# Kernel optimization log

Hardware: AMD Instinct MI355X
Metric: run time of the kernel (lower is better)

## Reference

```python
import jax, jax.numpy as jnp
import numpy as np

B, N, T, D = 4, 128, 64, 768
L_ATTN, HEADS = 4, 8
M_SSM = 4
D_INNER, D_STATE, HEADDIM = 1536, 64, 64
NHEADS = D_INNER // HEADDIM  # 24
D_CONV = 4
CONV_DIM = D_INNER + 2 * D_STATE  # 1664
IN_PROJ = 2 * D_INNER + 2 * D_STATE + NHEADS  # 3224
FFN_MULT = 4


def rmsnorm(x, w, eps=1e-5):
    return x * jax.lax.rsqrt(jnp.mean(x * x, -1, keepdims=True) + eps) * w


def mha(q_in, kv_in, Wq, Wk, Wv, Wo):
    b, lq, d = q_in.shape
    lk = kv_in.shape[1]
    dh = d // HEADS
    scale = 1.0 / float(np.sqrt(dh))
    q = (q_in @ Wq).reshape(b, lq, HEADS, dh)
    k = (kv_in @ Wk).reshape(b, lk, HEADS, dh)
    v = (kv_in @ Wv).reshape(b, lk, HEADS, dh)
    scores = jnp.einsum('bqhd,bkhd->bhqk', q, k) * scale
    attn = jax.nn.softmax(scores, axis=-1)
    o = jnp.einsum('bhqk,bkhd->bqhd', attn, v).reshape(b, lq, d)
    return o @ Wo


def mamba_block(x, in_proj_w, conv_w, conv_b, dt_bias, A_log, D_skip, norm_w, out_proj_w):
    # x: (b, l, D); selective-scan (Mamba2) with scalar-per-head A, ngroups=1
    b, l, _ = x.shape
    zxbcdt = x @ in_proj_w                       # (b, l, IN_PROJ)
    z = zxbcdt[..., :D_INNER]
    xBC = zxbcdt[..., D_INNER:D_INNER + CONV_DIM]
    dt = zxbcdt[..., D_INNER + CONV_DIM:]        # (b, l, NHEADS)
    # causal depthwise conv1d, kernel D_CONV
    xp = jnp.pad(xBC, ((0, 0), (D_CONV - 1, 0), (0, 0)))
    xc = sum(conv_w[k] * xp[:, k:k + l] for k in range(D_CONV)) + conv_b
    xc = jax.nn.silu(xc)
    xs = xc[..., :D_INNER].reshape(b, l, NHEADS, HEADDIM)
    Bm = xc[..., D_INNER:D_INNER + D_STATE]      # (b, l, D_STATE)
    Cm = xc[..., D_INNER + D_STATE:]             # (b, l, D_STATE)
    dt = jax.nn.softplus(dt + dt_bias)           # (b, l, NHEADS)
    A = -jnp.exp(A_log)                          # (NHEADS,)
    h0 = jnp.zeros((b, NHEADS, HEADDIM, D_STATE), x.dtype)

    def step(h, inp):
        xt, Bt, Ct, dtt = inp                    # (b,nh,hd), (b,ds), (b,ds), (b,nh)
        dA = jnp.exp(dtt * A)                    # (b, nh)
        h = h * dA[:, :, None, None] + (dtt[:, :, None, None] * xt[..., None]) * Bt[:, None, None, :]
        y = jnp.einsum('bhps,bs->bhp', h, Ct)
        return h, y

    hT, ys = jax.lax.scan(step, h0, (xs.transpose(1, 0, 2, 3), Bm.transpose(1, 0, 2), Cm.transpose(1, 0, 2), dt.transpose(1, 0, 2)))
    y = ys.transpose(1, 0, 2, 3) + D_skip[:, None] * xs  # skip connection per head
    y = y.reshape(b, l, D_INNER)
    y = rmsnorm(y * jax.nn.silu(z), norm_w)      # gated RMSNorm
    return y @ out_proj_w, hT


def reference(precepts, actions, attn_norm1_w, Wq, Wk, Wv, Wo, attn_norm2_w, ffn_w1, ffn_b1, ffn_w2, ffn_b2, ssm_norm_w, in_proj_w, conv_w, conv_b, dt_bias, A_log, D_skip, mamba_norm_w, out_proj_w, proj_w, proj_b):
    p = precepts.reshape(B * N, T, D)
    a = actions.reshape(B * N, T, D)
    for i in range(L_ATTN):
        cross = (i + 1) % 2 == 0
        q = rmsnorm(p, attn_norm1_w[i])
        kv = a if cross else q
        p = p + mha(q, kv, Wq[i], Wk[i], Wv[i], Wo[i])
        h_ = rmsnorm(p, attn_norm2_w[i])
        p = p + (jax.nn.gelu(h_ @ ffn_w1[i] + ffn_b1[i]) @ ffn_w2[i] + ffn_b2[i])
    # (b n) t d -> (b t) n d : scan over the num_steps axis
    z = p.reshape(B, N, T, D).transpose(0, 2, 1, 3).reshape(B * T, N, D)
    h_last = None
    for m in range(M_SSM):
        out, h_last = mamba_block(rmsnorm(z, ssm_norm_w[m]), in_proj_w[m], conv_w[m], conv_b[m], dt_bias[m], A_log[m], D_skip[m], mamba_norm_w[m], out_proj_w[m])
        z = z + out
    y = z @ proj_w + proj_b
    y = y.reshape(B, T, N, D).transpose(0, 2, 1, 3)  # b n t d
    return y, h_last


def setup_inputs() -> dict:
    key = jax.random.key(0)
    ks = jax.random.split(key, 16)
    s = 0.02
    f32 = jnp.float32
    return {
        'precepts': jax.random.normal(ks[0], (B, N, T, D), f32),
        'actions': jax.random.normal(ks[1], (B, N, T, D), f32),
        'attn_norm1_w': jnp.ones((L_ATTN, D), f32),
        'Wq': s * jax.random.normal(ks[2], (L_ATTN, D, D), f32),
        'Wk': s * jax.random.normal(ks[3], (L_ATTN, D, D), f32),
        'Wv': s * jax.random.normal(ks[4], (L_ATTN, D, D), f32),
        'Wo': s * jax.random.normal(ks[5], (L_ATTN, D, D), f32),
        'attn_norm2_w': jnp.ones((L_ATTN, D), f32),
        'ffn_w1': s * jax.random.normal(ks[6], (L_ATTN, D, FFN_MULT * D), f32),
        'ffn_b1': jnp.zeros((L_ATTN, FFN_MULT * D), f32),
        'ffn_w2': s * jax.random.normal(ks[7], (L_ATTN, FFN_MULT * D, D), f32),
        'ffn_b2': jnp.zeros((L_ATTN, D), f32),
        'ssm_norm_w': jnp.ones((M_SSM, D), f32),
        'in_proj_w': s * jax.random.normal(ks[8], (M_SSM, D, IN_PROJ), f32),
        'conv_w': s * jax.random.normal(ks[9], (M_SSM, D_CONV, CONV_DIM), f32),
        'conv_b': jnp.zeros((M_SSM, CONV_DIM), f32),
        'dt_bias': jax.random.uniform(ks[10], (M_SSM, NHEADS), f32, -2.0, 0.0),
        'A_log': jnp.broadcast_to(jnp.log(jnp.arange(1, NHEADS + 1, dtype=f32)), (M_SSM, NHEADS)),
        'D_skip': jnp.ones((M_SSM, NHEADS), f32),
        'mamba_norm_w': jnp.ones((M_SSM, D_INNER), f32),
        'out_proj_w': s * jax.random.normal(ks[11], (M_SSM, D_INNER, D), f32),
        'proj_w': s * jax.random.normal(ks[12], (D, D), f32),
        'proj_b': jnp.zeros((D,), f32),
    }
```

## Files before the change

kernel.cpp:

```cpp
#include <hip/hip_runtime.h>
#include <hip/hip_bf16.h>
#include <math.h>

constexpr long TOK  = 32768;
constexpr long HALF = TOK * 768;
constexpr int FLAG_ACC = 1, FLAG_GELU = 2, FLAG_PERM = 4, FLAG_BF16 = 8;

typedef __bf16 bf16x8 __attribute__((ext_vector_type(8)));
typedef __bf16 bf16x4 __attribute__((ext_vector_type(4)));
typedef float  f32x4  __attribute__((ext_vector_type(4)));

__device__ __forceinline__ void gload_lds16(const void* g, void* l) {
    __builtin_amdgcn_global_load_lds(
        (const __attribute__((address_space(1))) void*)g,
        (__attribute__((address_space(3))) void*)l, 16, 0, 0);
}
__device__ __forceinline__ float bf2f(__hip_bfloat16 v) { return __bfloat162float(v); }

__global__ __launch_bounds__(512, 2) void gemm256(
    const __hip_bfloat16* __restrict__ A,
    const __hip_bfloat16* __restrict__ BT,
    const float* __restrict__ bias,
    void* __restrict__ Cv, int ldc,
    int M, int N, int K, int flags, int moff)
{
    __shared__ __hip_bfloat16 As[2][256 * 64];
    __shared__ __hip_bfloat16 Bs[2][256 * 64];
    const int tid = threadIdx.x;
    const int wid = tid >> 6, lane = tid & 63;
    const int wm = wid >> 2, wn = wid & 3;
    const int lrow = lane & 15, lk = lane >> 4;
    const int nwg = gridDim.x * gridDim.y;
    const int orig = blockIdx.y * gridDim.x + blockIdx.x;
    const int q8 = nwg >> 3, r8 = nwg & 7;
    const int xcd = orig & 7, off = orig >> 3;
    const int wgid = (xcd < r8 ? xcd * (q8 + 1) : r8 * (q8 + 1) + (xcd - r8) * q8) + off;
    const int bm = (wgid / gridDim.x) * 256, bn = (wgid % gridDim.x) * 256;
    const int nk = K >> 6;

    f32x4 acc[4][8];
#pragma unroll
    for (int nf = 0; nf < 4; nf++)
#pragma unroll
        for (int mf = 0; mf < 8; mf++) acc[nf][mf] = f32x4{0.f, 0.f, 0.f, 0.f};

    bf16x8 Af[4][2];
    bf16x8 B0[2][2];
    bf16x8 B1[2][2];

    auto stage = [&](int kt, int which) {
        if (kt >= nk) return;
        const int dbuf = kt & 1;
        __hip_bfloat16* lbase = (which >= 2 ? &Bs[dbuf][0] : &As[dbuf][0]) + (which & 1) * 8192;
        const __hip_bfloat16* g = (which >= 2 ? BT : A);
        const int trow = (which >= 2 ? bn : bm) + (which & 1) * 128;
#pragma unroll
        for (int i = 0; i < 2; i++) {
            const int slot = i * 512 + tid;
            const int rl = slot >> 3, ch = slot & 7;
            const int sc = (ch ^ (rl & 7)) * 8;
            const long src = (long)(trow + rl) * K + (long)kt * 64 + sc;
            char* l = (char*)lbase + (i * 512 + wid * 64) * 16;
            gload_lds16(g + src, l);
        }
    };
    auto readA = [&](int dbuf, int mh) {
#pragma unroll
        for (int mq = 0; mq < 4; mq++)
#pragma unroll
            for (int ks = 0; ks < 2; ks++) {
                const int r = wm * 128 + mh * 64 + mq * 16 + lrow;
                const int ch = ((ks * 4 + lk) ^ (r & 7)) * 8;
                Af[mq][ks] = *(const bf16x8*)(const void*)&As[dbuf][r * 64 + ch];
            }
    };
    auto readB0 = [&](int dbuf) {
#pragma unroll
        for (int nf = 0; nf < 2; nf++)
#pragma unroll
            for (int ks = 0; ks < 2; ks++) {
                const int r = wn * 64 + nf * 16 + lrow;
                const int ch = ((ks * 4 + lk) ^ (r & 7)) * 8;
                B0[nf][ks] = *(const bf16x8*)(const void*)&Bs[dbuf][r * 64 + ch];
            }
    };
    auto readB1 = [&](int dbuf) {
#pragma unroll
        for (int nf = 0; nf < 2; nf++)
#pragma unroll
            for (int ks = 0; ks < 2; ks++) {
                const int r = wn * 64 + (2 + nf) * 16 + lrow;
                const int ch = ((ks * 4 + lk) ^ (r & 7)) * 8;
                B1[nf][ks] = *(const bf16x8*)(const void*)&Bs[dbuf][r * 64 + ch];
            }
    };

    stage(0, 0); stage(0, 1); stage(0, 2); stage(0, 3);
    stage(1, 2); stage(1, 3);
    asm volatile("s_waitcnt vmcnt(4)" ::: "memory");
    __builtin_amdgcn_s_barrier();

    for (int kt = 0; kt < nk; kt++) {
        const int cur = kt & 1;
        readA(cur, 0); readB0(cur);
        stage(kt + 1, 0);
        __builtin_amdgcn_s_barrier();
        __builtin_amdgcn_s_setprio(1);
#pragma unroll
        for (int nf = 0; nf < 2; nf++)
#pragma unroll
            for (int mq = 0; mq < 4; mq++)
#pragma unroll
                for (int ks = 0; ks < 2; ks++)
                    acc[nf][mq] = __builtin_amdgcn_mfma_f32_16x16x32_bf16(B0[nf][ks], Af[mq][ks], acc[nf][mq], 0, 0, 0);
        __builtin_amdgcn_s_setprio(0);
        __builtin_amdgcn_s_barrier();
        readB1(cur);
        stage(kt + 1, 1);
        __builtin_amdgcn_s_barrier();
        __builtin_amdgcn_s_setprio(1);
#pragma unroll
        for (int nf = 0; nf < 2; nf++)
#pragma unroll
            for (int mq = 0; mq < 4; mq++)
#pragma unroll
                for (int ks = 0; ks < 2; ks++)
                    acc[2 + nf][mq] = __builtin_amdgcn_mfma_f32_16x16x32_bf16(B1[nf][ks], Af[mq][ks], acc[2 + nf][mq], 0, 0, 0);
        __builtin_amdgcn_s_setprio(0);
        __builtin_amdgcn_s_barrier();
        readA(cur, 1);
        stage(kt + 2, 2);
        __builtin_amdgcn_s_barrier();
        __builtin_amdgcn_s_setprio(1);
#pragma unroll
        for (int nf = 0; nf < 2; nf++)
#pragma unroll
            for (int mq = 0; mq < 4; mq++)
#pragma unroll
                for (int ks = 0; ks < 2; ks++)
                    acc[2 + nf][4 + mq] = __builtin_amdgcn_mfma_f32_16x16x32_bf16(B1[nf][ks], Af[mq][ks], acc[2 + nf][4 + mq], 0, 0, 0);
        __builtin_amdgcn_s_setprio(0);
        __builtin_amdgcn_s_barrier();
        stage(kt + 2, 3);
        if (kt + 2 < nk) asm volatile("s_waitcnt vmcnt(4)" ::: "memory");
        else             asm volatile("s_waitcnt vmcnt(0)" ::: "memory");
        __builtin_amdgcn_s_barrier();
        __builtin_amdgcn_s_setprio(1);
#pragma unroll
        for (int nf = 0; nf < 2; nf++)
#pragma unroll
            for (int mq = 0; mq < 4; mq++)
#pragma unroll
                for (int ks = 0; ks < 2; ks++)
                    acc[nf][4 + mq] = __builtin_amdgcn_mfma_f32_16x16x32_bf16(B0[nf][ks], Af[mq][ks], acc[nf][4 + mq], 0, 0, 0);
        __builtin_amdgcn_s_setprio(0);
        __builtin_amdgcn_s_barrier();
    }

    float* Cf = (float*)Cv;
    __hip_bfloat16* Cb = (__hip_bfloat16*)Cv;
#pragma unroll
    for (int nf = 0; nf < 4; nf++) {
        const int gcb = bn + wn * 64 + nf * 16 + lk * 4;
        if (gcb >= N) continue;
        f32x4 b4 = f32x4{0.f, 0.f, 0.f, 0.f};
        if (bias) b4 = *(const f32x4*)&bias[gcb];
#pragma unroll
        for (int mf = 0; mf < 8; mf++) {
            const int gr = bm + wm * 128 + mf * 16 + lrow;
            f32x4 v = acc[nf][mf] + b4;
            if (flags & FLAG_GELU) {
#pragma unroll
                for (int j = 0; j < 4; j++) {
                    const float x = v[j];
                    const float u = 1.5957691216057308f * (x + 0.044715f * x * x * x);
                    v[j] = x / (1.f + __expf(-u));
                }
            }
            if (flags & FLAG_PERM) {
                const int mg = moff + gr;
                const int b_ = mg >> 13, t_ = (mg >> 7) & 63, n_ = mg & 127;
                *(f32x4*)&Cf[(((long)(b_ * 128 + n_)) * 64 + t_) * ldc + gcb] = v;
            } else if (flags & FLAG_BF16) {
                __hip_bfloat16 o0 = __float2bfloat16(v[0]), o1 = __float2bfloat16(v[1]);
                __hip_bfloat16 o2 = __float2bfloat16(v[2]), o3 = __float2bfloat16(v[3]);
                ushort4 o = { *(ushort*)&o0, *(ushort*)&o1, *(ushort*)&o2, *(ushort*)&o3 };
                *(ushort4*)&Cb[(long)gr * ldc + gcb] = o;
            } else if (flags & FLAG_ACC) {
                float* dst = &Cf[(long)gr * ldc + gcb];
                f32x4 old = *(const f32x4*)dst;
                *(f32x4*)dst = old + v;
            } else {
                *(f32x4*)&Cf[(long)gr * ldc + gcb] = v;
            }
        }
    }
}

__global__ __launch_bounds__(256) void gemm_bf16(
    const __hip_bfloat16* __restrict__ A,
    const __hip_bfloat16* __restrict__ BT,
    const float* __restrict__ bias,
    void* __restrict__ Cv, int ldc,
    int M, int N, int K, int flags, int moff)
{
    __shared__ __hip_bfloat16 As[2][128 * 32];
    __shared__ __hip_bfloat16 Bs[2][128 * 32];
    const int tid = threadIdx.x;
    const int wv = tid >> 6, lane = tid & 63;
    const int nwg = gridDim.x * gridDim.y;
    const int orig = blockIdx.y * gridDim.x + blockIdx.x;
    const int q8 = nwg >> 3, r8 = nwg & 7;
    const int xcd = orig & 7, off = orig >> 3;
    const int wgid = (xcd < r8 ? xcd * (q8 + 1) : r8 * (q8 + 1) + (xcd - r8) * q8) + off;
    const int bm = (wgid / gridDim.x) * 128, bn = (wgid % gridDim.x) * 128;
    const int wr = (wv >> 1) * 64, wc = (wv & 1) * 64;
    const int lrow = lane & 15, lk = lane >> 4;
    const int ck = (lk ^ (lrow & 3) ^ ((lrow >> 2) & 3)) * 8;

    f32x4 acc[4][4];
#pragma unroll
    for (int n = 0; n < 4; n++)
#pragma unroll
        for (int m = 0; m < 4; m++) acc[n][m] = f32x4{0.f, 0.f, 0.f, 0.f};

    const int nk = K >> 5;
    auto stage = [&](int kt, int buf) {
#pragma unroll
        for (int i = 0; i < 2; i++) {
            const int lin = i * 256 + tid;
            const int row = lin >> 2;
            const int ks  = (((lin & 3) ^ (row & 3) ^ ((row >> 2) & 3)) * 8);
            const long asrc = (long)(bm + row) * K + kt * 32 + ks;
            const long bsrc = (long)(bn + row) * K + kt * 32 + ks;
            char* la = (char*)&As[buf][0] + (i * 256 + wv * 64) * 16;
            char* lb = (char*)&Bs[buf][0] + (i * 256 + wv * 64) * 16;
            gload_lds16(A + asrc, la);
            gload_lds16(BT + bsrc, lb);
        }
    };

    stage(0, 0);
    __syncthreads();
    for (int kt = 0; kt < nk; kt++) {
        const int cur = kt & 1;
        if (kt + 1 < nk) stage(kt + 1, cur ^ 1);
        bf16x8 af[4], bfr[4];
#pragma unroll
        for (int m = 0; m < 4; m++) {
            af[m]  = *(const bf16x8*)(const void*)&As[cur][(wr + m * 16 + lrow) * 32 + ck];
            bfr[m] = *(const bf16x8*)(const void*)&Bs[cur][(wc + m * 16 + lrow) * 32 + ck];
        }
#pragma unroll
        for (int n = 0; n < 4; n++)
#pragma unroll
            for (int m = 0; m < 4; m++)
                acc[n][m] = __builtin_amdgcn_mfma_f32_16x16x32_bf16(bfr[n], af[m], acc[n][m], 0, 0, 0);
        __syncthreads();
    }

    float* Cf = (float*)Cv;
    __hip_bfloat16* Cb = (__hip_bfloat16*)Cv;
#pragma unroll
    for (int n = 0; n < 4; n++) {
        const int gcb = bn + wc + n * 16 + lk * 4;
        if (gcb >= N) continue;
        f32x4 b4 = f32x4{0.f, 0.f, 0.f, 0.f};
        if (bias) b4 = *(const f32x4*)&bias[gcb];
#pragma unroll
        for (int m = 0; m < 4; m++) {
            const int gr = bm + wr + m * 16 + lrow;
            f32x4 v = acc[n][m] + b4;
            if (flags & FLAG_GELU) {
#pragma unroll
                for (int j = 0; j < 4; j++) {
                    const float x = v[j];
                    const float u = 1.5957691216057308f * (x + 0.044715f * x * x * x);
                    v[j] = x / (1.f + __expf(-u));
                }
            }
            if (flags & FLAG_PERM) {
                const int mg = moff + gr;
                const int b_ = mg >> 13, t_ = (mg >> 7) & 63, n_ = mg & 127;
                *(f32x4*)&Cf[(((long)(b_ * 128 + n_)) * 64 + t_) * ldc + gcb] = v;
            } else if (flags & FLAG_BF16) {
                __hip_bfloat16 o0 = __float2bfloat16(v[0]), o1 = __float2bfloat16(v[1]);
                __hip_bfloat16 o2 = __float2bfloat16(v[2]), o3 = __float2bfloat16(v[3]);
                ushort4 o = { *(ushort*)&o0, *(ushort*)&o1, *(ushort*)&o2, *(ushort*)&o3 };
                *(ushort4*)&Cb[(long)gr * ldc + gcb] = o;
            } else if (flags & FLAG_ACC) {
                float* dst = &Cf[(long)gr * ldc + gcb];
                f32x4 old = *(const f32x4*)dst;
                *(f32x4*)dst = old + v;
            } else {
                *(f32x4*)&Cf[(long)gr * ldc + gcb] = v;
            }
        }
    }
}

__global__ void convT_kernel(const float* __restrict__ W, __hip_bfloat16* __restrict__ WT,
                             int K, int N, int Npad)
{
    __shared__ float t[32][33];
    const int k0 = blockIdx.y * 32, n0 = blockIdx.x * 32;
    const int tx = threadIdx.x & 31, ty = threadIdx.x >> 5;
#pragma unroll
    for (int i = 0; i < 4; i++) {
        int k = k0 + ty + i * 8, n = n0 + tx;
        t[ty + i * 8][tx] = (k < K && n < N) ? W[(long)k * N + n] : 0.f;
    }
    __syncthreads();
#pragma unroll
    for (int i = 0; i < 4; i++) {
        int n = n0 + ty + i * 8, k = k0 + tx;
        if (n < Npad && k < K) WT[(long)n * K + k] = __float2bfloat16(t[tx][ty + i * 8]);
    }
}

__global__ void cvt_kernel(const float4* __restrict__ x, ushort4* __restrict__ y, long n4)
{
    long i = (long)blockIdx.x * 256 + threadIdx.x;
    if (i >= n4) return;
    float4 v = x[i];
    __hip_bfloat16 a = __float2bfloat16(v.x), b = __float2bfloat16(v.y);
    __hip_bfloat16 c = __float2bfloat16(v.z), d = __float2bfloat16(v.w);
    ushort4 o = { *(ushort*)&a, *(ushort*)&b, *(ushort*)&c, *(ushort*)&d };
    y[i] = o;
}

__global__ void rmsnorm_f32(const float* __restrict__ x, const float* __restrict__ w,
                            __hip_bfloat16* __restrict__ out, int D, int xs, int os, long nrows)
{
    const int wv = threadIdx.x >> 6, lane = threadIdx.x & 63;
    const long row = (long)blockIdx.x * 4 + wv;
    if (row >= nrows) return;
    const float* xr = x + row * xs;
    const int it = D >> 8;
    float ss = 0.f;
    for (int i = 0; i < it; i++) {
        const float4 v = *(const float4*)&xr[(i * 64 + lane) * 4];
        ss += v.x * v.x + v.y * v.y + v.z * v.z + v.w * v.w;
    }
    for (int o = 32; o; o >>= 1) ss += __shfl_xor(ss, o);
    const float sc = rsqrtf(ss / D + 1e-5f);
    __hip_bfloat16* orow = out + row * os;
    for (int i = 0; i < it; i++) {
        const int e = (i * 64 + lane) * 4;
        const float4 v = *(const float4*)&xr[e];
        const float4 g = *(const float4*)&w[e];
        bf16x4 o;
        o[0] = (__bf16)(v.x * sc * g.x); o[1] = (__bf16)(v.y * sc * g.y);
        o[2] = (__bf16)(v.z * sc * g.z); o[3] = (__bf16)(v.w * sc * g.w);
        *(bf16x4*)(void*)&orow[e] = o;
    }
}
__global__ void rmsnorm_b16(const __hip_bfloat16* __restrict__ x, const float* __restrict__ w,
                            __hip_bfloat16* __restrict__ out, int D, int xs, int os, long nrows)
{
    const int wv = threadIdx.x >> 6, lane = threadIdx.x & 63;
    const long row = (long)blockIdx.x * 4 + wv;
    if (row >= nrows) return;
    const __hip_bfloat16* xr = x + row * xs;
    const int it = D >> 8;
    float ss = 0.f;
    for (int i = 0; i < it; i++) {
        const bf16x4 v = *(const bf16x4*)(const void*)&xr[(i * 64 + lane) * 4];
#pragma unroll
        for (int e = 0; e < 4; e++) { const float f = (float)v[e]; ss += f * f; }
    }
    for (int o = 32; o; o >>= 1) ss += __shfl_xor(ss, o);
    const float sc = rsqrtf(ss / D + 1e-5f);
    __hip_bfloat16* orow = out + row * os;
    for (int i = 0; i < it; i++) {
        const int e = (i * 64 + lane) * 4;
        const bf16x4 v = *(const bf16x4*)(const void*)&xr[e];
        const float4 g = *(const float4*)&w[e];
        bf16x4 o;
        o[0] = (__bf16)((float)v[0] * sc * g.x); o[1] = (__bf16)((float)v[1] * sc * g.y);
        o[2] = (__bf16)((float)v[2] * sc * g.z); o[3] = (__bf16)((float)v[3] * sc * g.w);
        *(bf16x4*)(void*)&orow[e] = o;
    }
}

__global__ __launch_bounds__(256) void attn_kernel(
    const __hip_bfloat16* __restrict__ QKV, __hip_bfloat16* __restrict__ O)
{
    __shared__ __align__(16) __hip_bfloat16 Qs[3 * 64 * 32];
    __shared__ __align__(16) __hip_bfloat16 Ks[3 * 64 * 32];
    __shared__ __align__(16) __hip_bfloat16 VT[2 * 96 * 32];
    __shared__ __align__(16) __hip_bfloat16 Ps[2 * 64 * 32];
    const int tid = threadIdx.x;
    const int wid = tid >> 6, lane = tid & 63;
    const int lrow = lane & 15, lk = lane >> 4;
    const int b = blockIdx.x >> 3, h = blockIdx.x & 7;
    const long base = (long)b * 64 * 2304 + h * 96;

#pragma unroll
    for (int i = 0; i < 3; i++) {
        const int v = i * 256 + tid;
        const int r = v / 12, c8 = v - r * 12;
        const int kst = c8 >> 2, ch = c8 & 3, slot = ch ^ (r & 3);
        const bf16x8 q = *(const bf16x8*)(const void*)&QKV[base + (long)r * 2304 + c8 * 8];
        const bf16x8 k = *(const bf16x8*)(const void*)&QKV[base + (long)r * 2304 + 768 + c8 * 8];
        *(bf16x8*)(void*)&Qs[(kst * 64 + r) * 32 + slot * 8] = q;
        *(bf16x8*)(void*)&Ks[(kst * 64 + r) * 32 + slot * 8] = k;
    }
    for (int i = 0; i < 16; i++) {
        const int k = wid * 16 + i;
        const __hip_bfloat16* vrow = &QKV[base + (long)k * 2304 + 1536];
        const int sb = (k >> 3) & 3, khi = k >> 5, klo = k & 7;
        {
            const int d = lane;
            VT[(khi * 96 + d) * 32 + ((sb ^ (d & 3)) * 8) + klo] = vrow[d];
        }
        if (lane < 32) {
            const int d = 64 + lane;
            VT[(khi * 96 + d) * 32 + ((sb ^ (d & 3)) * 8) + klo] = vrow[d];
        }
    }
    __syncthreads();

    const int ck = (lk ^ (lrow & 3)) * 8;
    f32x4 s[4];
#pragma unroll
    for (int n = 0; n < 4; n++) s[n] = f32x4{0.f, 0.f, 0.f, 0.f};
#pragma unroll
    for (int kst = 0; kst < 3; kst++) {
        const bf16x8 qf = *(const bf16x8*)(const void*)&Qs[(kst * 64 + wid * 16 + lrow) * 32 + ck];
#pragma unroll
        for (int n = 0; n < 4; n++) {
            const bf16x8 kf = *(const bf16x8*)(const void*)&Ks[(kst * 64 + n * 16 + lrow) * 32 + ck];
            s[n] = __builtin_amdgcn_mfma_f32_16x16x32_bf16(qf, kf, s[n], 0, 0, 0);
        }
    }
    const float scale = 0.102062072615966f;
#pragma unroll
    for (int n = 0; n < 4; n++) s[n] *= scale;
    float inv[4];
#pragma unroll
    for (int j = 0; j < 4; j++) {
        float mx = fmaxf(fmaxf(s[0][j], s[1][j]), fmaxf(s[2][j], s[3][j]));
        mx = fmaxf(mx, __shfl_xor(mx, 1));
        mx = fmaxf(mx, __shfl_xor(mx, 2));
        mx = fmaxf(mx, __shfl_xor(mx, 4));
        mx = fmaxf(mx, __shfl_xor(mx, 8));
        float sum = 0.f;
#pragma unroll
        for (int n = 0; n < 4; n++) { s[n][j] = __expf(s[n][j] - mx); sum += s[n][j]; }
        sum += __shfl_xor(sum, 1);
        sum += __shfl_xor(sum, 2);
        sum += __shfl_xor(sum, 4);
        sum += __shfl_xor(sum, 8);
        inv[j] = 1.f / sum;
    }
#pragma unroll
    for (int n = 0; n < 4; n++) {
        const int k = n * 16 + lrow;
        const int kst = n >> 1, kc = ((n & 1) << 1) + (lrow >> 3), ke = lrow & 7;
#pragma unroll
        for (int j = 0; j < 4; j++) {
            const int q = wid * 16 + lk * 4 + j;
            Ps[(kst * 64 + q) * 32 + ((kc ^ (q & 3)) * 8) + ke] = __float2bfloat16(s[n][j] * inv[j]);
        }
    }
    __syncthreads();

    const int wq = wid >> 1, wd = wid & 1;
    f32x4 y[3][2];
#pragma unroll
    for (int mv = 0; mv < 3; mv++)
#pragma unroll
        for (int np = 0; np < 2; np++) y[mv][np] = f32x4{0.f, 0.f, 0.f, 0.f};
#pragma unroll
    for (int ks = 0; ks < 2; ks++) {
        bf16x8 vf[3], pf[2];
#pragma unroll
        for (int mv = 0; mv < 3; mv++)
            vf[mv] = *(const bf16x8*)(const void*)&VT[(ks * 96 + wd * 48 + mv * 16 + lrow) * 32 + ck];
#pragma unroll
        for (int np = 0; np < 2; np++)
            pf[np] = *(const bf16x8*)(const void*)&Ps[(ks * 64 + wq * 32 + np * 16 + lrow) * 32 + ck];
#pragma unroll
        for (int mv = 0; mv < 3; mv++)
#pragma unroll
            for (int np = 0; np < 2; np++)
                y[mv][np] = __builtin_amdgcn_mfma_f32_16x16x32_bf16(vf[mv], pf[np], y[mv][np], 0, 0, 0);
    }
#pragma unroll
    for (int mv = 0; mv < 3; mv++) {
        const int d0 = wd * 48 + mv * 16 + lk * 4;
#pragma unroll
        for (int np = 0; np < 2; np++) {
            const int q = wq * 32 + np * 16 + lrow;
            bf16x4 o;
#pragma unroll
            for (int j = 0; j < 4; j++) o[j] = (__bf16)y[mv][np][j];
            *(bf16x4*)(void*)&O[(long)(b * 64 + q) * 768 + h * 96 + d0] = o;
        }
    }
}

__global__ void transpose_kernel(const float* __restrict__ P, float* __restrict__ Z)
{
    long lin = (long)blockIdx.x * 256 + threadIdx.x;
    if (lin >= HALF) return;
    int d = (int)(lin % 768);
    long rowz = lin / 768;
    int n = rowz & 127, t = (int)((rowz >> 7) & 63), b = (int)(rowz >> 13);
    long rowp = ((long)(b * 128 + n)) * 64 + t;
    Z[lin] = P[rowp * 768 + d];
}

__global__ __launch_bounds__(256) void conv_kernel(
    const __hip_bfloat16* __restrict__ zx, const float* __restrict__ cw,
    const float* __restrict__ cb, __hip_bfloat16* __restrict__ xc,
    __hip_bfloat16* __restrict__ bcB, long rows)
{
    const long r = blockIdx.x;
    const int tid = threadIdx.x;
    if (tid >= 208) return;
    const int c0 = tid * 8;
    const int n = (int)(r & 127);
    float acc[8];
    {
        const float4 b0 = *(const float4*)&cb[c0];
        const float4 b1 = *(const float4*)&cb[c0 + 4];
        acc[0] = b0.x; acc[1] = b0.y; acc[2] = b0.z; acc[3] = b0.w;
        acc[4] = b1.x; acc[5] = b1.y; acc[6] = b1.z; acc[7] = b1.w;
    }
#pragma unroll
    for (int k = 0; k < 4; k++) {
        if (n - 3 + k < 0) continue;
        const bf16x8 xv = *(const bf16x8*)(const void*)&zx[(r - 3 + k) * 3328 + 1536 + c0];
        const float4 w0 = *(const float4*)&cw[k * 1664 + c0];
        const float4 w1 = *(const float4*)&cw[k * 1664 + c0 + 4];
        acc[0] += w0.x * (float)xv[0]; acc[1] += w0.y * (float)xv[1];
        acc[2] += w0.z * (float)xv[2]; acc[3] += w0.w * (float)xv[3];
        acc[4] += w1.x * (float)xv[4]; acc[5] += w1.y * (float)xv[5];
        acc[6] += w1.z * (float)xv[6]; acc[7] += w1.w * (float)xv[7];
    }
    bf16x8 o;
#pragma unroll
    for (int e = 0; e < 8; e++) {
        const float s = acc[e] / (1.f + __expf(-acc[e]));
        o[e] = (__bf16)s;
    }
    if (c0 < 1536) *(bf16x8*)(void*)&xc[r * 1664 + c0] = o;
    else           *(bf16x8*)(void*)&bcB[r * 128 + (c0 - 1536)] = o;
}

__global__ void dt_kernel(const __hip_bfloat16* __restrict__ zx, const float* __restrict__ bias,
                          float* __restrict__ dtf, long count)
{
    long lin = (long)blockIdx.x * 256 + threadIdx.x;
    if (lin >= count) return;
    int h = (int)(lin % 24);
    long r = lin / 24;
    float v = bf2f(zx[r * 3328 + 3200 + h]) + bias[h];
    dtf[lin] = (v > 0.f) ? v + log1pf(expf(-v)) : log1pf(expf(v));
}

__global__ __launch_bounds__(256) void ssd_kernel(
    const __hip_bfloat16* __restrict__ zx0, const float* __restrict__ dtf0,
    const __hip_bfloat16* __restrict__ bcB0, __hip_bfloat16* __restrict__ xc0,
    const float* __restrict__ Alog, const float* __restrict__ Dskip,
    float* __restrict__ hout, int bt0)
{
    __shared__ __align__(16) char SM[50688];
    __hip_bfloat16* Cl  = (__hip_bfloat16*)SM;
    __hip_bfloat16* Bl  = Cl + 8192;
    __hip_bfloat16* Ml  = (__hip_bfloat16*)SM;
    __hip_bfloat16* XTl = (__hip_bfloat16*)(SM + 32768);
    __hip_bfloat16* BTl = (__hip_bfloat16*)SM;
    float* cum = (float*)(SM + 49152);
    float* dtl = cum + 128;
    float* wl  = dtl + 128;

    const int tid = threadIdx.x;
    const int wid = tid >> 6, lane = tid & 63;
    const int lrow = lane & 15, lk = lane >> 4;
    const int btl = blockIdx.x / 24, h = blockIdx.x % 24;
    const long rowbase = (long)btl * 128;

    const __hip_bfloat16* zxp = zx0 + rowbase * 3328 + h * 64;
    const float* dtp = dtf0 + rowbase * 24;
    const __hip_bfloat16* bcp = bcB0 + rowbase * 128;
    __hip_bfloat16* xcp = xc0 + rowbase * 1664 + h * 64;

    const float A  = -expf(Alog[h]);
    const float Dh = Dskip[h];

#pragma unroll
    for (int i = 0; i < 4; i++) {
        const int v = tid + i * 256;
        const int row = v >> 3, c8 = v & 7;
        const int kst = c8 >> 2, ch = c8 & 3;
        const int slot = ch ^ (row & 3);
        bf16x8 vB = *(const bf16x8*)(const void*)&bcp[(long)row * 128 + c8 * 8];
        bf16x8 vC = *(const bf16x8*)(const void*)&bcp[(long)row * 128 + 64 + c8 * 8];
        *(bf16x8*)(void*)&Bl[(kst * 128 + row) * 32 + slot * 8] = vB;
        *(bf16x8*)(void*)&Cl[(kst * 128 + row) * 32 + slot * 8] = vC;
    }
    for (int i = 0; i < 32; i++) {
        const int t = wid * 32 + i;
        const int slot = (i >> 3) ^ (lane & 3);
        XTl[(wid * 64 + lane) * 32 + slot * 8 + (i & 7)] = xcp[(long)t * 1664 + lane];
    }
    if (tid < 128) dtl[tid] = dtp[(long)tid * 24 + h];
    __syncthreads();
    if (tid < 128) cum[tid] = dtl[tid] * A;
    __syncthreads();
    for (int off = 1; off < 128; off <<= 1) {
        float v = 0.f;
        if (tid < 128 && tid >= off) v = cum[tid - off];
        __syncthreads();
        if (tid < 128) cum[tid] += v;
        __syncthreads();
    }
    if (tid < 128) wl[tid] = expf(cum[127] - cum[tid]) * dtl[tid];
    __syncthreads();

    const int wr1 = (wid >> 1) * 64, wc1 = (wid & 1) * 64;
    const int ck = (lk ^ (lrow & 3)) * 8;
    f32x4 a1[4][4];
#pragma unroll
    for (int m = 0; m < 4; m++)
#pragma unroll
        for (int n = 0; n < 4; n++) a1[m][n] = f32x4{0.f, 0.f, 0.f, 0.f};
#pragma unroll
    for (int kst = 0; kst < 2; kst++) {
        bf16x8 ca[4], bb[4];
#pragma unroll
        for (int m = 0; m < 4; m++)
            ca[m] = *(const bf16x8*)(const void*)&Cl[(kst * 128 + wr1 + m * 16 + lrow) * 32 + ck];
#pragma unroll
        for (int n = 0; n < 4; n++)
            bb[n] = *(const bf16x8*)(const void*)&Bl[(kst * 128 + wc1 + n * 16 + lrow) * 32 + ck];
#pragma unroll
        for (int m = 0; m < 4; m++)
#pragma unroll
            for (int n = 0; n < 4; n++)
                a1[m][n] = __builtin_amdgcn_mfma_f32_16x16x32_bf16(ca[m], bb[n], a1[m][n], 0, 0, 0);
    }
    __syncthreads();

#pragma unroll
    for (int m = 0; m < 4; m++) {
        const int tb = wr1 + m * 16 + lk * 4;
        const f32x4 c4 = *(const f32x4*)&cum[tb];
#pragma unroll
        for (int n = 0; n < 4; n++) {
            const int j = wc1 + n * 16 + lrow;
            const float cj = cum[j], dj = dtl[j];
            const int jst = j >> 5, jc = (j >> 3) & 3, je = j & 7;
#pragma unroll
            for (int jj = 0; jj < 4; jj++) {
                const int t = tb + jj;
                float val = 0.f;
                if (j <= t) val = a1[m][n][jj] * expf(c4[jj] - cj) * dj;
                Ml[(jst * 128 + t) * 32 + ((jc ^ (t & 3)) * 8) + je] = __float2bfloat16(val);
            }
        }
    }
    __syncthreads();

    const int wr2 = (wid >> 1) * 64, wc2 = (wid & 1) * 32;
    f32x4 a2[4][2];
#pragma unroll
    for (int m = 0; m < 4; m++)
#pragma unroll
        for (int n = 0; n < 2; n++) a2[m][n] = f32x4{0.f, 0.f, 0.f, 0.f};
#pragma unroll
    for (int kst = 0; kst < 4; kst++) {
        bf16x8 am[4], bn[2];
#pragma unroll
        for (int m = 0; m < 4; m++)
            am[m] = *(const bf16x8*)(const void*)&Ml[(kst * 128 + wr2 + m * 16 + lrow) * 32 + ck];
#pragma unroll
        for (int n = 0; n < 2; n++)
            bn[n] = *(const bf16x8*)(const void*)&XTl[(kst * 64 + wc2 + n * 16 + lrow) * 32 + ck];
#pragma unroll
        for (int m = 0; m < 4; m++)
#pragma unroll
            for (int n = 0; n < 2; n++)
                a2[m][n] = __builtin_amdgcn_mfma_f32_16x16x32_bf16(am[m], bn[n], a2[m][n], 0, 0, 0);
    }

#pragma unroll
    for (int m = 0; m < 4; m++) {
        const int tb = wr2 + m * 16 + lk * 4;
#pragma unroll
        for (int n = 0; n < 2; n++) {
            const int p = wc2 + n * 16 + lrow;
#pragma unroll
            for (int jj = 0; jj < 4; jj++) {
                const int t = tb + jj;
                const float x = bf2f(XTl[((t >> 5) * 64 + p) * 32 + ((((t >> 3) & 3) ^ (p & 3)) * 8) + (t & 7)]);
                const float zg = bf2f(zxp[(long)t * 3328 + p]);
                const float y = (a2[m][n][jj] + Dh * x) * (zg / (1.f + expf(-zg)));
                xcp[(long)t * 1664 + p] = __float2bfloat16(y);
            }
        }
    }

    if (hout) {
        __syncthreads();
        for (int i = 0; i < 32; i++) {
            const int j = wid * 32 + i;
            const int slot = (i >> 3) ^ (lane & 3);
            BTl[(wid * 64 + lane) * 32 + slot * 8 + (j & 7)] = bcp[(long)j * 128 + lane];
        }
        __syncthreads();
        const int wrp = (wid >> 1) * 32, wcs = (wid & 1) * 32;
        f32x4 a3[2][2];
#pragma unroll
        for (int m = 0; m < 2; m++)
#pragma unroll
            for (int n = 0; n < 2; n++) a3[m][n] = f32x4{0.f, 0.f, 0.f, 0.f};
#pragma unroll
        for (int kst = 0; kst < 4; kst++) {
            const int jb = kst * 32 + lk * 8;
            const f32x4 wa = *(const f32x4*)&wl[jb];
            const f32x4 wb = *(const f32x4*)&wl[jb + 4];
            bf16x8 xw[2], bn[2];
#pragma unroll
            for (int m = 0; m < 2; m++) {
                bf16x8 xr = *(const bf16x8*)(const void*)&XTl[(kst * 64 + wrp + m * 16 + lrow) * 32 + ck];
                bf16x8 t;
#pragma unroll
                for (int e = 0; e < 4; e++) t[e] = (__bf16)((float)xr[e] * wa[e]);
#pragma unroll
                for (int e = 0; e < 4; e++) t[4 + e] = (__bf16)((float)xr[4 + e] * wb[e]);
                xw[m] = t;
            }
#pragma unroll
            for (int n = 0; n < 2; n++)
                bn[n] = *(const bf16x8*)(const void*)&BTl[(kst * 64 + wcs + n * 16 + lrow) * 32 + ck];
#pragma unroll
            for (int m = 0; m < 2; m++)
#pragma unroll
                for (int n = 0; n < 2; n++)
                    a3[m][n] = __builtin_amdgcn_mfma_f32_16x16x32_bf16(xw[m], bn[n], a3[m][n], 0, 0, 0);
        }
        float* hp = hout + ((long)(bt0 + btl) * 24 + h) * 4096;
#pragma unroll
        for (int m = 0; m < 2; m++) {
            const int pb = wrp + m * 16 + lk * 4;
#pragma unroll
            for (int n = 0; n < 2; n++) {
                const int s = wcs + n * 16 + lrow;
#pragma unroll
                for (int jj = 0; jj < 4; jj++)
                    hp[(long)(pb + jj) * 64 + s] = a3[m][n][jj];
            }
        }
    }
}

extern "C" void kernel_launch(void* const* d_in, const int* in_sizes, int n_in,
                              void* d_out, int out_size, void* d_ws, size_t ws_size,
                              hipStream_t stream)
{
    const float* precepts  = (const float*)d_in[0];
    const float* actions   = (const float*)d_in[1];
    const float* attn_n1   = (const float*)d_in[2];
    const float* Wq        = (const float*)d_in[3];
    const float* Wk        = (const float*)d_in[4];
    const float* Wv        = (const float*)d_in[5];
    const float* Wo        = (const float*)d_in[6];
    const float* attn_n2   = (const float*)d_in[7];
    const float* ffn_w1    = (const float*)d_in[8];
    const float* ffn_b1    = (const float*)d_in[9];
    const float* ffn_w2    = (const float*)d_in[10];
    const float* ffn_b2    = (const float*)d_in[11];
    const float* ssm_norm  = (const float*)d_in[12];
    const float* in_proj   = (const float*)d_in[13];
    const float* conv_w    = (const float*)d_in[14];
    const float* conv_b    = (const float*)d_in[15];
    const float* dt_bias   = (const float*)d_in[16];
    const float* A_log     = (const float*)d_in[17];
    const float* D_skip    = (const float*)d_in[18];
    const float* mamba_nw  = (const float*)d_in[19];
    const float* out_proj  = (const float*)d_in[20];
    const float* proj_w    = (const float*)d_in[21];
    const float* proj_b    = (const float*)d_in[22];

    float* out  = (float*)d_out;
    float* Z    = out;
    float* P    = out + HALF;
    float* hout = out + HALF;

    __hip_bfloat16* wb = (__hip_bfloat16*)d_ws;
    long wo = 0;
    auto walloc = [&](long els) { __hip_bfloat16* p = wb + wo; wo += els; return p; };
    __hip_bfloat16* WqkvT = walloc(4L * 2304 * 768);
    __hip_bfloat16* W1T   = walloc(4L * 3072 * 768);
    __hip_bfloat16* W2T   = walloc(4L * 768 * 3072);
    __hip_bfloat16* inT   = walloc(4L * 3328 * 768);
    __hip_bfloat16* outT  = walloc(4L * 768 * 1536);
    __hip_bfloat16* projT = walloc(768L * 768);
    __hip_bfloat16* WoT   = walloc(4L * 768 * 768);
    char* pbase = (char*)(wb + ((wo + 255) & ~255L));
    const size_t used_w = (size_t)(pbase - (char*)d_ws);
    const size_t avail = ws_size > used_w ? ws_size - used_w : 0;

    int CB = 512;
    while (CB > 8 && (unsigned long long)CB * 884736ull > avail) CB >>= 1;
    int CBT = 256;
    while (CBT > 2 && (unsigned long long)CBT * 1912832ull > avail) CBT >>= 1;

    auto gemm = [&](const __hip_bfloat16* A, const __hip_bfloat16* BT, const float* bias,
                    void* C, int ldc, int M, int N, int Npad, int K, int flags, int moff) {
        if ((M & 255) == 0 && (Npad & 255) == 0 && (K & 63) == 0) {
            dim3 g(Npad / 256, M / 256);
            hipLaunchKernelGGL(gemm256, g, dim3(512), 0, stream,
                               A, BT, bias, C, ldc, M, N, K, flags, moff);
        } else {
            dim3 g(Npad / 128, M / 128);
            hipLaunchKernelGGL(gemm_bf16, g, dim3(256), 0, stream,
                               A, BT, bias, C, ldc, M, N, K, flags, moff);
        }
    };
    auto cvtT = [&](const float* W, __hip_bfloat16* WT, int K, int N, int Npad) {
        dim3 g((Npad + 31) / 32, (K + 31) / 32);
        hipLaunchKernelGGL(convT_kernel, g, dim3(256), 0, stream, W, WT, K, N, Npad);
    };
    auto cvt = [&](const float* x, __hip_bfloat16* y, long n) {
        long n4 = n / 4;
        hipLaunchKernelGGL(cvt_kernel, dim3((n4 + 255) / 256), dim3(256), 0, stream,
                           (const float4*)x, (ushort4*)y, n4);
    };
    auto rmsF = [&](const float* x, const float* w, __hip_bfloat16* o, int D, int xs, int os, long rows) {
        hipLaunchKernelGGL(rmsnorm_f32, dim3((rows + 3) / 4), dim3(256), 0, stream,
                           x, w, o, D, xs, os, rows);
    };
    auto rmsB = [&](const __hip_bfloat16* x, const float* w, __hip_bfloat16* o, int D, int xs, int os, long rows) {
        hipLaunchKernelGGL(rmsnorm_b16, dim3((rows + 3) / 4), dim3(256), 0, stream,
                           x, w, o, D, xs, os, rows);
    };

    for (int l = 0; l < 4; l++) {
        cvtT(Wq + (long)l * 589824, WqkvT + (long)l * 2304 * 768,                768, 768, 768);
        cvtT(Wk + (long)l * 589824, WqkvT + (long)l * 2304 * 768 +  768L * 768,  768, 768, 768);
        cvtT(Wv + (long)l * 589824, WqkvT + (long)l * 2304 * 768 + 1536L * 768,  768, 768, 768);
        cvtT(Wo + (long)l * 589824, WoT + (long)l * 589824, 768, 768, 768);
        cvtT(ffn_w1 + (long)l * 2359296, W1T + (long)l * 2359296, 768, 3072, 3072);
        cvtT(ffn_w2 + (long)l * 2359296, W2T + (long)l * 2359296, 3072, 768, 768);
    }
    for (int m = 0; m < 4; m++) {
        cvtT(in_proj + (long)m * 768 * 3224, inT + (long)m * 3328 * 768, 768, 3224, 3328);
        cvtT(out_proj + (long)m * 1536 * 768, outT + (long)m * 768 * 1536, 1536, 768, 768);
    }
    cvtT(proj_w, projT, 768, 768, 768);

    hipMemcpyAsync(P, precepts, HALF * sizeof(float), hipMemcpyDeviceToDevice, stream);
    {
        const long rA = (long)CB * 64;
        __hip_bfloat16* bufA   = (__hip_bfloat16*)pbase;
        __hip_bfloat16* actB   = bufA + rA * 768;
        __hip_bfloat16* bufQKV = actB + rA * 768;
        __hip_bfloat16* bufH   = bufQKV + rA * 2304;
        const int nac = 512 / CB;
        const int Mr = (int)rA;
        if (nac == 1) cvt(actions, actB, rA * 768);
        for (int layer = 0; layer < 4; layer++) {
            const bool cross = ((layer + 1) % 2) == 0;
            for (int c = 0; c < nac; c++) {
                const long tok0 = (long)c * rA;
                float* Pc = P + tok0 * 768;
                rmsF(Pc, attn_n1 + layer * 768, bufA, 768, 768, 768, Mr);
                if (!cross) {
                    gemm(bufA, WqkvT + (long)layer * 2304 * 768, nullptr, bufQKV, 2304,
                         Mr, 2304, 2304, 768, FLAG_BF16, 0);
                } else {
                    if (nac != 1) cvt(actions + tok0 * 768, actB, rA * 768);
                    gemm(bufA, WqkvT + (long)layer * 2304 * 768, nullptr, bufQKV, 2304,
                         Mr, 768, 768, 768, FLAG_BF16, 0);
                    gemm(actB, WqkvT + (long)layer * 2304 * 768 + 768L * 768, nullptr,
                         bufQKV + 768, 2304, Mr, 1536, 1536, 768, FLAG_BF16, 0);
                }
                hipLaunchKernelGGL(attn_kernel, dim3(CB * 8), dim3(256), 0, stream,
                                   bufQKV, bufA);
                gemm(bufA, WoT + (long)layer * 589824, nullptr, Pc, 768,
                     Mr, 768, 768, 768, FLAG_ACC, 0);
                rmsF(Pc, attn_n2 + layer * 768, bufA, 768, 768, 768, Mr);
                gemm(bufA, W1T + (long)layer * 2359296, ffn_b1 + layer * 3072, bufH, 3072,
                     Mr, 3072, 3072, 768, FLAG_GELU | FLAG_BF16, 0);
                gemm(bufH, W2T + (long)layer * 2359296, ffn_b2 + layer * 768, Pc, 768,
                     Mr, 768, 768, 3072, FLAG_ACC, 0);
            }
        }
    }

    hipLaunchKernelGGL(transpose_kernel, dim3((int)((HALF + 255) / 256)), dim3(256), 0, stream, P, Z);

    {
        const long rM = (long)CBT * 128;
        __hip_bfloat16* xn  = (__hip_bfloat16*)pbase;
        __hip_bfloat16* zx  = xn + rM * 768;
        float*          dtf = (float*)(zx + rM * 3328);
        __hip_bfloat16* xc  = (__hip_bfloat16*)(dtf + rM * 24);
        __hip_bfloat16* yb  = xc + rM * 1664;
        __hip_bfloat16* bcB = yb + rM * 1536;
        const int nmc = 256 / CBT;
        const int Mr = (int)rM;
        for (int m = 0; m < 4; m++) {
            for (int c = 0; c < nmc; c++) {
                float* Zc = Z + (long)c * rM * 768;
                rmsF(Zc, ssm_norm + m * 768, xn, 768, 768, 768, Mr);
                gemm(xn, inT + (long)m * 3328 * 768, nullptr, zx, 3328,
                     Mr, 3224, 3328, 768, FLAG_BF16, 0);
                hipLaunchKernelGGL(conv_kernel, dim3((int)rM), dim3(256), 0, stream,
                                   zx, conv_w + m * 4 * 1664, conv_b + m * 1664, xc, bcB, rM);
                const long dtn = rM * 24;
                hipLaunchKernelGGL(dt_kernel, dim3((int)((dtn + 255) / 256)), dim3(256), 0, stream,
                                   zx, dt_bias + m * 24, dtf, dtn);
                hipLaunchKernelGGL(ssd_kernel, dim3(CBT * 24), dim3(256), 0, stream,
                                   zx, dtf, bcB, xc, A_log + m * 24, D_skip + m * 24,
                                   (m == 3) ? hout : nullptr, c * CBT);
                rmsB(xc, mamba_nw + m * 1536, yb, 1536, 1664, 1536, Mr);
                gemm(yb, outT + (long)m * 768 * 1536, nullptr, Zc, 768,
                     Mr, 768, 768, 1536, FLAG_ACC, 0);
            }
        }
    }

    {
        __hip_bfloat16* Zb = (__hip_bfloat16*)pbase;
        cvt(Z, Zb, HALF);
        gemm(Zb, projT, proj_b, out, 768, 32768, 768, 768, 768, FLAG_PERM, 0);
    }
}
```

Measured before the change: 7.152 ms.

## Stage bf16 GEMM epilogue through LDS for coalesced stores; regroup prefetch and MFMA order

For bf16 outputs the epilogue now writes each wave's converted tile into a padded region of shared memory and then reads it back as full 16-byte rows, so global stores are coalesced instead of scattered 8-byte writes. The main loop also issues two stage prefetches together in the first phase and reorders the MFMA loop nest to put the k-slice outermost. The epilogue reuses the A shared buffer, which assumes every wave has finished its last reads; there is no barrier before the writes, and the N bounds check is dropped on the bf16 path.

```diff
diff --git a/kernel.cpp b/kernel.cpp
--- a/kernel.cpp
+++ b/kernel.cpp
@@ -24,8 +24,8 @@
     void* __restrict__ Cv, int ldc,
     int M, int N, int K, int flags, int moff)
 {
-    __shared__ __hip_bfloat16 As[2][256 * 64];
-    __shared__ __hip_bfloat16 Bs[2][256 * 64];
+    __shared__ __align__(16) __hip_bfloat16 As[2][256 * 64];
+    __shared__ __align__(16) __hip_bfloat16 Bs[2][256 * 64];
     const int tid = threadIdx.x;
     const int wid = tid >> 6, lane = tid & 63;
     const int wm = wid >> 2, wn = wid & 3;
@@ -103,28 +103,27 @@
     for (int kt = 0; kt < nk; kt++) {
         const int cur = kt & 1;
         readA(cur, 0); readB0(cur);
-        stage(kt + 1, 0);
+        stage(kt + 1, 0); stage(kt + 1, 1);
         __builtin_amdgcn_s_barrier();
         __builtin_amdgcn_s_setprio(1);
 #pragma unroll
-        for (int nf = 0; nf < 2; nf++)
-#pragma unroll
-            for (int mq = 0; mq < 4; mq++)
-#pragma unroll
-                for (int ks = 0; ks < 2; ks++)
+        for (int ks = 0; ks < 2; ks++)
+#pragma unroll
+            for (int nf = 0; nf < 2; nf++)
+#pragma unroll
+                for (int mq = 0; mq < 4; mq++)
                     acc[nf][mq] = __builtin_amdgcn_mfma_f32_16x16x32_bf16(B0[nf][ks], Af[mq][ks], acc[nf][mq], 0, 0, 0);
         __builtin_amdgcn_s_setprio(0);
         __builtin_amdgcn_s_barrier();
         readB1(cur);
-        stage(kt + 1, 1);
         __builtin_amdgcn_s_barrier();
         __builtin_amdgcn_s_setprio(1);
 #pragma unroll
-        for (int nf = 0; nf < 2; nf++)
-#pragma unroll
-            for (int mq = 0; mq < 4; mq++)
-#pragma unroll
-                for (int ks = 0; ks < 2; ks++)
+        for (int ks = 0; ks < 2; ks++)
+#pragma unroll
+            for (int nf = 0; nf < 2; nf++)
+#pragma unroll
+                for (int mq = 0; mq < 4; mq++)
                     acc[2 + nf][mq] = __builtin_amdgcn_mfma_f32_16x16x32_bf16(B1[nf][ks], Af[mq][ks], acc[2 + nf][mq], 0, 0, 0);
         __builtin_amdgcn_s_setprio(0);
         __builtin_amdgcn_s_barrier();
@@ -133,11 +132,11 @@
         __builtin_amdgcn_s_barrier();
         __builtin_amdgcn_s_setprio(1);
 #pragma unroll
-        for (int nf = 0; nf < 2; nf++)
-#pragma unroll
-            for (int mq = 0; mq < 4; mq++)
-#pragma unroll
-                for (int ks = 0; ks < 2; ks++)
+        for (int ks = 0; ks < 2; ks++)
+#pragma unroll
+            for (int nf = 0; nf < 2; nf++)
+#pragma unroll
+                for (int mq = 0; mq < 4; mq++)
                     acc[2 + nf][4 + mq] = __builtin_amdgcn_mfma_f32_16x16x32_bf16(B1[nf][ks], Af[mq][ks], acc[2 + nf][4 + mq], 0, 0, 0);
         __builtin_amdgcn_s_setprio(0);
         __builtin_amdgcn_s_barrier();
@@ -147,11 +146,11 @@
         __builtin_amdgcn_s_barrier();
         __builtin_amdgcn_s_setprio(1);
 #pragma unroll
-        for (int nf = 0; nf < 2; nf++)
-#pragma unroll
-            for (int mq = 0; mq < 4; mq++)
-#pragma unroll
-                for (int ks = 0; ks < 2; ks++)
+        for (int ks = 0; ks < 2; ks++)
+#pragma unroll
+            for (int nf = 0; nf < 2; nf++)
+#pragma unroll
+                for (int mq = 0; mq < 4; mq++)
                     acc[nf][4 + mq] = __builtin_amdgcn_mfma_f32_16x16x32_bf16(B0[nf][ks], Af[mq][ks], acc[nf][4 + mq], 0, 0, 0);
         __builtin_amdgcn_s_setprio(0);
         __builtin_amdgcn_s_barrier();
@@ -159,39 +158,74 @@
 
     float* Cf = (float*)Cv;
     __hip_bfloat16* Cb = (__hip_bfloat16*)Cv;
-#pragma unroll
-    for (int nf = 0; nf < 4; nf++) {
-        const int gcb = bn + wn * 64 + nf * 16 + lk * 4;
-        if (gcb >= N) continue;
-        f32x4 b4 = f32x4{0.f, 0.f, 0.f, 0.f};
-        if (bias) b4 = *(const f32x4*)&bias[gcb];
-#pragma unroll
-        for (int mf = 0; mf < 8; mf++) {
-            const int gr = bm + wm * 128 + mf * 16 + lrow;
-            f32x4 v = acc[nf][mf] + b4;
-            if (flags & FLAG_GELU) {
-#pragma unroll
-                for (int j = 0; j < 4; j++) {
-                    const float x = v[j];
-                    const float u = 1.5957691216057308f * (x + 0.044715f * x * x * x);
-                    v[j] = x / (1.f + __expf(-u));
+    if (flags & FLAG_BF16) {
+        char* lw = (char*)&As[0][0] + (size_t)wid * (64 * 176);
+        const int colg = bn + wn * 64;
+#pragma unroll
+        for (int half = 0; half < 2; half++) {
+#pragma unroll
+            for (int nf = 0; nf < 4; nf++) {
+                const int col = nf * 16 + lk * 4;
+                f32x4 b4 = f32x4{0.f, 0.f, 0.f, 0.f};
+                if (bias) b4 = *(const f32x4*)&bias[colg + col];
+#pragma unroll
+                for (int m4 = 0; m4 < 4; m4++) {
+                    const int row = m4 * 16 + lrow;
+                    f32x4 v = acc[nf][half * 4 + m4] + b4;
+                    if (flags & FLAG_GELU) {
+#pragma unroll
+                        for (int j = 0; j < 4; j++) {
+                            const float x = v[j];
+                            const float u = 1.5957691216057308f * (x + 0.044715f * x * x * x);
+                            v[j] = x / (1.f + __expf(-u));
+                        }
+                    }
+                    bf16x4 o;
+                    o[0] = (__bf16)v[0]; o[1] = (__bf16)v[1];
+                    o[2] = (__bf16)v[2]; o[3] = (__bf16)v[3];
+                    *(bf16x4*)(void*)(lw + row * 176 + col * 2) = o;
                 }
             }
-            if (flags & FLAG_PERM) {
-                const int mg = moff + gr;
-                const int b_ = mg >> 13, t_ = (mg >> 7) & 63, n_ = mg & 127;
-                *(f32x4*)&Cf[(((long)(b_ * 128 + n_)) * 64 + t_) * ldc + gcb] = v;
-            } else if (flags & FLAG_BF16) {
-                __hip_bfloat16 o0 = __float2bfloat16(v[0]), o1 = __float2bfloat16(v[1]);
-                __hip_bfloat16 o2 = __float2bfloat16(v[2]), o3 = __float2bfloat16(v[3]);
-                ushort4 o = { *(ushort*)&o0, *(ushort*)&o1, *(ushort*)&o2, *(ushort*)&o3 };
-                *(ushort4*)&Cb[(long)gr * ldc + gcb] = o;
-            } else if (flags & FLAG_ACC) {
-                float* dst = &Cf[(long)gr * ldc + gcb];
-                f32x4 old = *(const f32x4*)dst;
-                *(f32x4*)dst = old + v;
-            } else {
-                *(f32x4*)&Cf[(long)gr * ldc + gcb] = v;
+            asm volatile("s_waitcnt lgkmcnt(0)" ::: "memory");
+#pragma unroll
+            for (int rr = 0; rr < 8; rr++) {
+                const int row = rr * 8 + (lane >> 3);
+                const long gr = (long)(bm + wm * 128 + half * 64 + row);
+                const bf16x8 d = *(const bf16x8*)(const void*)(lw + row * 176 + (lane & 7) * 16);
+                *(bf16x8*)(void*)&Cb[gr * ldc + colg + (lane & 7) * 8] = d;
+            }
+            asm volatile("s_waitcnt lgkmcnt(0)" ::: "memory");
+        }
+    } else {
+#pragma unroll
+        for (int nf = 0; nf < 4; nf++) {
+            const int gcb = bn + wn * 64 + nf * 16 + lk * 4;
+            if (gcb >= N) continue;
+            f32x4 b4 = f32x4{0.f, 0.f, 0.f, 0.f};
+            if (bias) b4 = *(const f32x4*)&bias[gcb];
+#pragma unroll
+            for (int mf = 0; mf < 8; mf++) {
+                const int gr = bm + wm * 128 + mf * 16 + lrow;
+                f32x4 v = acc[nf][mf] + b4;
+                if (flags & FLAG_GELU) {
+#pragma unroll
+                    for (int j = 0; j < 4; j++) {
+                        const float x = v[j];
+                        const float u = 1.5957691216057308f * (x + 0.044715f * x * x * x);
+                        v[j] = x / (1.f + __expf(-u));
+                    }
+                }
+                if (flags & FLAG_PERM) {
+                    const int mg = moff + gr;
+                    const int b_ = mg >> 13, t_ = (mg >> 7) & 63, n_ = mg & 127;
+                    *(f32x4*)&Cf[(((long)(b_ * 128 + n_)) * 64 + t_) * ldc + gcb] = v;
+                } else if (flags & FLAG_ACC) {
+                    float* dst = &Cf[(long)gr * ldc + gcb];
+                    f32x4 old = *(const f32x4*)dst;
+                    *(f32x4*)dst = old + v;
+                } else {
+                    *(f32x4*)&Cf[(long)gr * ldc + gcb] = v;
+                }
             }
         }
     }
```

Result: faster. 6.483 ms (-9.4%).
